# Performance work log

Hardware: AMD Instinct MI355X
Metric: run time of the kernel (lower is better)

## Reference

```python
import jax, jax.numpy as jnp
import numpy as np
from jax import lax

DEPTH = 8
LEAK = 0.01  # activations.relu(x, 0.01) == leaky relu


def _lrelu(z):
    return jnp.where(z >= 0, z, LEAK * z)


def _forward(x, mask, bucket_size, W_emb, b_emb, W, U, b, W1, b1,
             W_action_1, U_action_1, b_action_1, W_action_3, b_action_3):
    S = int(bucket_size)
    B = x.shape[0]
    H = W_emb.shape[1]
    dm = mask.T[:S]                         # [S,B] data mask (float)
    xe = x @ W_emb + b_emb                  # [B,S,H] embedding
    xe = jnp.transpose(xe, (1, 0, 2))[:S]   # [S,B,H] time-major
    # last_value_mask: 1 only at the final time step
    lvm = jnp.concatenate([jnp.zeros((S - 1, B), jnp.float32),
                           jnp.ones((1, B), jnp.float32)], axis=0)

    def hstep(carry, seq):
        h_tm1, nm_tm1, hv_tm1 = carry
        xt, pm, phv, lv = seq
        # action MLP -> per-sample gate
        a = _lrelu(xt @ W_action_1 + h_tm1 @ U_action_1 + b_action_1)  # [B,A]
        nm = jnp.clip(0.2 * (a @ W_action_3 + b_action_3) + 0.5, 0.0, 1.0)[:, 0]  # hard_sigmoid
        nm = (1.0 - lv) * (pm * phv * nm)
        both = pm * phv * (1.0 - nm) * hv_tm1
        x_only = pm * phv * (nm + (1.0 - nm) * (1.0 - hv_tm1))
        h_only = (1.0 - pm + pm * (1.0 - phv)) * (1.0 - nm) * hv_tm1
        hv = both + x_only + h_only
        h_ = _lrelu(xt @ W + h_tm1 @ U + b)      # [B,inner]
        h_ = _lrelu(h_ @ W1 + b1)                # [B,H]
        h = both[:, None] * h_ + x_only[:, None] * xt + h_only[:, None] * h_tm1
        return (h, nm, hv), (h, nm, hv)

    def vstep(carry, _):
        xv, xm, phv = carry  # [S,B,H], [S,B], [S,B]
        init = (jnp.zeros((B, H), jnp.float32),
                jnp.ones((B,), jnp.float32),
                jnp.zeros((B,), jnp.float32))
        _, (hs, nms, hvs) = lax.scan(hstep, init, (xv, xm, phv, lvm))
        # shift new_mask left by one step, pad last step with ones
        nms = jnp.concatenate([nms[1:], jnp.ones((1, B), jnp.float32)], axis=0)
        return (hs, nms, hvs), None

    (hfin, _, _), _ = lax.scan(vstep, (xe, dm, dm), None, length=DEPTH - 1)
    return hfin[-1]  # [B,H]: last time step of the last vertical level


def setup_inputs() -> dict:
    key = jax.random.key(0)
    ks = jax.random.split(key, 9)
    B, S, IN, H, INNER, A = 64, 256, 256, 256, 512, 64
    g = lambda k, shp: jax.random.normal(k, shp, jnp.float32) * np.float32(np.sqrt(2.0 / (shp[0] + shp[1])))
    return {
        "x": jax.random.normal(ks[0], (B, S, IN), jnp.float32),
        "mask": jnp.ones((B, S), jnp.float32),
        "bucket_size": S,
        "W_emb": g(ks[1], (IN, H)),
        "b_emb": jnp.zeros((H,), jnp.float32),
        "W": g(ks[2], (H, INNER)),
        "U": g(ks[3], (H, INNER)),
        "b": jnp.zeros((INNER,), jnp.float32),
        "W1": g(ks[4], (INNER, H)),
        "b1": jnp.zeros((H,), jnp.float32),
        "W_action_1": g(ks[5], (H, A)),
        "U_action_1": g(ks[6], (H, A)),
        "b_action_1": jnp.zeros((A,), jnp.float32),
        "W_action_3": g(ks[7], (A, 1)),
        "b_action_3": jnp.zeros((1,), jnp.float32),
    }


def reference(x, mask, bucket_size, W_emb, b_emb, W, U, b, W1, b1,
              W_action_1, U_action_1, b_action_1, W_action_3, b_action_3):
    return _forward(x, mask, bucket_size, W_emb, b_emb, W, U, b, W1, b1,
                    W_action_1, U_action_1, b_action_1, W_action_3, b_action_3)
```

## Files before the change

### kernel.cpp

```cpp
#include <hip/hip_runtime.h>
#include <stdint.h>


typedef _Float16 f16x8 __attribute__((ext_vector_type(8)));
typedef float    f32x4 __attribute__((ext_vector_type(4)));

static constexpr int SS = 256, BB = 64, DIN = 256, DH = 256, DNN = 512, DA = 64;
static constexpr int FS = 32;

static constexpr size_t OFF_FLAGS = 0;
static constexpr size_t OFF_WEMB  = 32768;
static constexpr size_t SZ_WEMB   = (size_t)DIN * DH * 2;
static constexpr size_t OFF_W     = OFF_WEMB + SZ_WEMB;
static constexpr size_t SZ_WU     = (size_t)DH * DNN * 2;
static constexpr size_t OFF_U     = OFF_W + SZ_WU;
static constexpr size_t OFF_W1    = OFF_U + SZ_WU;
static constexpr size_t SZ_W1     = (size_t)DNN * DH * 2;
static constexpr size_t OFF_WA1   = OFF_W1 + SZ_W1;
static constexpr size_t SZ_WA     = (size_t)DH * DA * 2;
static constexpr size_t OFF_UA1   = OFF_WA1 + SZ_WA;
static constexpr size_t OFF_NM    = OFF_UA1 + SZ_WA;
static constexpr size_t SZ_NM     = (size_t)SS * BB * 4;
static constexpr size_t OFF_HV    = OFF_NM + 8 * SZ_NM;
static constexpr size_t OFF_HB    = (size_t)4 << 20;
static constexpr size_t SZ_HB     = (size_t)SS * BB * DH * 2;
static constexpr size_t WS_NEEDED = OFF_HB + 8 * SZ_HB;

__device__ __forceinline__ float lrelu(float v) { return v >= 0.0f ? v : 0.01f * v; }

__device__ __forceinline__ f32x4 ld128(const f32x4* p) {
  f32x4 r;
  asm volatile("global_load_dwordx4 %0, %1, off sc0 sc1" : "=v"(r) : "v"(p) : "memory");
  return r;
}
__device__ __forceinline__ void st128(f32x4* p, f32x4 v) {
  asm volatile("global_store_dwordx4 %0, %1, off sc0 sc1" :: "v"(p), "v"(v) : "memory");
}
__device__ __forceinline__ float ldf(const float* p) {
  float r;
  asm volatile("global_load_dword %0, %1, off sc0 sc1" : "=v"(r) : "v"(p) : "memory");
  return r;
}
__device__ __forceinline__ void stf(float* p, float v) {
  asm volatile("global_store_dword %0, %1, off sc0 sc1" :: "v"(p), "v"(v) : "memory");
}
__device__ __forceinline__ void stu(unsigned* p, unsigned v) {
  asm volatile("global_store_dword %0, %1, off sc0 sc1" :: "v"(p), "v"(v) : "memory");
}
__device__ __forceinline__ void vwait() {
  asm volatile("s_waitcnt vmcnt(0)" ::: "memory");
  __builtin_amdgcn_sched_barrier(0);
}

__device__ __forceinline__ void pollf(const unsigned* p, unsigned need) {
  #pragma nounroll
  for (int g = 0; g < (1 << 18); ++g) {
    unsigned v;
    asm volatile("global_load_dword %0, %1, off sc0 sc1\n\ts_waitcnt vmcnt(0)"
                 : "=v"(v) : "v"(p) : "memory");
    if (v >= need) return;
    if (g > 64)     __builtin_amdgcn_s_sleep(2);
    else if (g > 8) __builtin_amdgcn_s_sleep(1);
  }
}

__global__ void zero_flags_k(unsigned* f) {
  #pragma unroll
  for (int i = 0; i < 8; ++i) f[threadIdx.x + 1024 * i] = 0u;
}

__global__ void pack_weight_k(const float* __restrict__ src, _Float16* __restrict__ dst,
                              int K, int N) {
  int idx = blockIdx.x * 256 + threadIdx.x;
  if (idx >= K * N) return;
  int k = idx / N, n = idx - k * N;
  int kt = k >> 5, q = (k >> 3) & 3, jj = k & 7;
  int nt = n >> 4, l = n & 15;
  size_t p = (((size_t)(kt * (N >> 4) + nt) * 4 + q) * 16 + l) * 8 + jj;
  dst[p] = (_Float16)src[idx];
}

__global__ __launch_bounds__(512, 2) void emb_k(const float* __restrict__ xin,
                                                const float* __restrict__ b_emb,
                                                char* __restrict__ ws) {
  const int tid = threadIdx.x, wave = tid >> 6, lane = tid & 63;
  const int l15 = lane & 15, quad = lane >> 4;
  const _Float16* Wp = (const _Float16*)(ws + OFF_WEMB);
  _Float16* xe = (_Float16*)(ws + OFF_HB);

  f16x8 bE[16];
  #pragma unroll
  for (int kt = 0; kt < 8; ++kt)
    #pragma unroll
    for (int i = 0; i < 2; ++i)
      bE[kt * 2 + i] = *(const f16x8*)(Wp + (((size_t)(kt * 16 + (wave * 2 + i)) * 4 + quad) * 16 + l15) * 8);
  float ber[2] = { b_emb[(wave * 2) * 16 + l15], b_emb[(wave * 2 + 1) * 16 + l15] };

  __shared__ __align__(16) _Float16 xtF[32 * 65 * 8];
  __shared__ __align__(16) _Float16 oF[32 * 65 * 8];

  for (int tt = 0; tt < 4; ++tt) {
    const int t = (int)blockIdx.x + 64 * tt;
    #pragma unroll
    for (int c = 0; c < 4; ++c) {
      int u = tid + 512 * c, s = u >> 5, kg = u & 31;
      const float* src = xin + ((size_t)s * SS + t) * DIN + kg * 8;
      f32x4 v0 = *(const f32x4*)src, v1 = *(const f32x4*)(src + 4);
      f16x8 p;
      p[0]=(_Float16)v0[0]; p[1]=(_Float16)v0[1]; p[2]=(_Float16)v0[2]; p[3]=(_Float16)v0[3];
      p[4]=(_Float16)v1[0]; p[5]=(_Float16)v1[1]; p[6]=(_Float16)v1[2]; p[7]=(_Float16)v1[3];
      *(f16x8*)(xtF + ((size_t)kg * 65 + s) * 8) = p;
    }
    __syncthreads();
    f32x4 acc[2][4] = {};
    #pragma unroll
    for (int kt = 0; kt < 8; ++kt) {
      f16x8 ax[4];
      #pragma unroll
      for (int mt = 0; mt < 4; ++mt)
        ax[mt] = *(const f16x8*)(xtF + (((size_t)(kt * 4 + quad)) * 65 + (mt * 16 + l15)) * 8);
      #pragma unroll
      for (int i = 0; i < 2; ++i)
        #pragma unroll
        for (int mt = 0; mt < 4; ++mt)
          acc[i][mt] = __builtin_amdgcn_mfma_f32_16x16x32_f16(ax[mt], bE[kt * 2 + i], acc[i][mt], 0, 0, 0);
    }
    #pragma unroll
    for (int i = 0; i < 2; ++i) {
      int n = (wave * 2 + i) * 16 + l15;
      int kq = n >> 3, jn = n & 7;
      #pragma unroll
      for (int mt = 0; mt < 4; ++mt)
        #pragma unroll
        for (int r = 0; r < 4; ++r) {
          int s = mt * 16 + quad * 4 + r;
          oF[((size_t)kq * 65 + s) * 8 + jn] = (_Float16)(acc[i][mt][r] + ber[i]);
        }
    }
    __syncthreads();
    #pragma unroll
    for (int c = 0; c < 4; ++c) {
      int u = tid + 512 * c, kq = u >> 6, s = u & 63;
      f32x4 v = *(const f32x4*)(oF + ((size_t)kq * 65 + s) * 8);
      *((f32x4*)(xe + (((size_t)t * 32 + kq) * 64 + s) * 8)) = v;
    }
    __syncthreads();
  }
}

__global__ __launch_bounds__(512, 2) void pipe_k(
    const float* __restrict__ mask, const float* __restrict__ b_in,
    const float* __restrict__ b1v, const float* __restrict__ bA1,
    const float* __restrict__ WA3, const float* __restrict__ bA3,
    char* __restrict__ ws, float* __restrict__ outp) {
  const int bId   = (int)blockIdx.x;
  const int level = 1 + (bId >> 2);
  const int g     = bId & 3;
  const int tid   = threadIdx.x, wave = tid >> 6, lane = tid & 63;
  const int l15   = lane & 15, quad = lane >> 4;
  const int kq16  = tid >> 4, sp16 = tid & 15;

  unsigned* flags = (unsigned*)(ws + OFF_FLAGS);
  unsigned* hfl   = flags + (size_t)(level * 4 + g) * FS;
  unsigned* hflP  = flags + (size_t)((level - 1) * 4 + g) * FS;

  const _Float16* Wp   = (const _Float16*)(ws + OFF_W);
  const _Float16* Up   = (const _Float16*)(ws + OFF_U);
  const _Float16* W1p  = (const _Float16*)(ws + OFF_W1);
  const _Float16* WA1p = (const _Float16*)(ws + OFF_WA1);
  const _Float16* UA1p = (const _Float16*)(ws + OFF_UA1);

  const f32x4* hPrev4 = (const f32x4*)((_Float16*)(ws + OFF_HB) + (size_t)(level - 1) * SS * BB * DH);
  f32x4*       hOwn4  = (f32x4*)((_Float16*)(ws + OFF_HB) + (size_t)level * SS * BB * DH);
  float*       nmW    = (float*)(ws + OFF_NM + (size_t)level * SZ_NM);
  float*       hvW    = (float*)(ws + OFF_HV + (size_t)level * SZ_NM);
  const float* nmR    = (const float*)(ws + OFF_NM + (size_t)(level - 1) * SZ_NM);
  const float* hvR    = (const float*)(ws + OFF_HV + (size_t)(level - 1) * SZ_NM);

  float bir[4];
  #pragma unroll
  for (int nt = 0; nt < 4; ++nt) bir[nt] = b_in[(wave * 4 + nt) * 16 + l15];
  float b1r[2];
  #pragma unroll
  for (int nt = 0; nt < 2; ++nt) b1r[nt] = b1v[(wave * 2 + nt) * 16 + l15];
  const float wa3r = WA3[(wave & 3) * 16 + l15];
  const float ba1r = bA1[(wave & 3) * 16 + l15];
  const float bA3v = bA3[0];

  __shared__ __align__(16) _Float16 xtL[32 * 16 * 8];
  __shared__ __align__(16) _Float16 hL [32 * 16 * 8];
  __shared__ __align__(16) _Float16 g1L[64 * 16 * 8];
  __shared__ float zL[64];
  __shared__ float gB[16], gX[16], gH[16], gHv[16];

  for (int i = tid; i < 32 * 16 * 8; i += 512) hL[i] = (_Float16)0;
  if (tid < 16) gHv[tid] = 0.0f;
  __syncthreads();

  if (level >= 2) pollf(hflP, 1);
  __syncthreads();
  {
    f32x4 v = ld128(hPrev4 + kq16 * 64 + g * 16 + sp16);
    vwait();
    ((f32x4*)xtL)[tid] = v;
  }
  __syncthreads();

  for (int t = 0; t < SS; ++t) {
    const bool last = (t == SS - 1);

    if (level >= 2) pollf(hflP, (unsigned)((t + 2 <= SS) ? (t + 2) : SS));

    {
      f32x4 acc[4] = {};
      #pragma unroll
      for (int kt = 0; kt < 8; ++kt) {
        f16x8 ax = *(const f16x8*)(xtL + ((size_t)((kt * 4 + quad) * 16 + l15)) * 8);
        f16x8 ah = *(const f16x8*)(hL  + ((size_t)((kt * 4 + quad) * 16 + l15)) * 8);
        #pragma unroll
        for (int i = 0; i < 4; ++i) {
          f16x8 wf = *(const f16x8*)(Wp + (((size_t)(kt * 32 + (wave * 4 + i)) * 4 + quad) * 16 + l15) * 8);
          f16x8 uf = *(const f16x8*)(Up + (((size_t)(kt * 32 + (wave * 4 + i)) * 4 + quad) * 16 + l15) * 8);
          acc[i] = __builtin_amdgcn_mfma_f32_16x16x32_f16(ax, wf, acc[i], 0, 0, 0);
          acc[i] = __builtin_amdgcn_mfma_f32_16x16x32_f16(ah, uf, acc[i], 0, 0, 0);
        }
      }
      #pragma unroll
      for (int i = 0; i < 4; ++i) {
        const int n = (wave * 4 + i) * 16 + l15;
        const int kqn = n >> 3, jn = n & 7;
        #pragma unroll
        for (int r = 0; r < 4; ++r)
          g1L[((size_t)kqn * 16 + (quad * 4 + r)) * 8 + jn] = (_Float16)lrelu(acc[i][r] + bir[i]);
      }
      if (wave < 4) {
        f32x4 aa = {};
        #pragma unroll
        for (int kt = 0; kt < 8; ++kt) {
          f16x8 ax = *(const f16x8*)(xtL + ((size_t)((kt * 4 + quad) * 16 + l15)) * 8);
          f16x8 ah = *(const f16x8*)(hL  + ((size_t)((kt * 4 + quad) * 16 + l15)) * 8);
          f16x8 wa = *(const f16x8*)(WA1p + (((size_t)(kt * 4 + wave) * 4 + quad) * 16 + l15) * 8);
          f16x8 ua = *(const f16x8*)(UA1p + (((size_t)(kt * 4 + wave) * 4 + quad) * 16 + l15) * 8);
          aa = __builtin_amdgcn_mfma_f32_16x16x32_f16(ax, wa, aa, 0, 0, 0);
          aa = __builtin_amdgcn_mfma_f32_16x16x32_f16(ah, ua, aa, 0, 0, 0);
        }
        #pragma unroll
        for (int r = 0; r < 4; ++r) {
          float v = lrelu(aa[r] + ba1r) * wa3r;
          v += __shfl_xor(v, 1); v += __shfl_xor(v, 2);
          v += __shfl_xor(v, 4); v += __shfl_xor(v, 8);
          if (l15 == 0) zL[wave * 16 + quad * 4 + r] = v;
        }
      }
    }
    __syncthreads();

    f32x4 c1[2] = {};
    #pragma unroll
    for (int kt = 0; kt < 16; ++kt) {
      f16x8 ag = *(const f16x8*)(g1L + ((size_t)((kt * 4 + quad) * 16 + l15)) * 8);
      #pragma unroll
      for (int nt = 0; nt < 2; ++nt) {
        f16x8 w1f = *(const f16x8*)(W1p + (((size_t)(kt * 16 + (wave * 2 + nt)) * 4 + quad) * 16 + l15) * 8);
        c1[nt] = __builtin_amdgcn_mfma_f32_16x16x32_f16(ag, w1f, c1[nt], 0, 0, 0);
      }
    }

    f32x4 pf;
    float pmv = 1.0f, phh = 0.0f;
    {
      const bool wantGate = (tid < 16) && (level >= 2);
      if (!last) pf = ld128(hPrev4 + (size_t)(t + 1) * 2048 + kq16 * 64 + g * 16 + sp16);
      if (wantGate) {
        size_t tn = (t + 1 < SS) ? (size_t)(t + 1) : 0;
        pmv = ldf(nmR + tn * BB + g * 16 + tid);
        phh = ldf(hvR + (size_t)t * BB + g * 16 + tid);
      }
      vwait();
      if (wantGate) asm volatile("" : "+v"(pmv), "+v"(phh));
    }

    if (tid < 16) {
      const int s = tid;
      float pm, phv;
      if (level == 1) {
        float mv = mask[(size_t)(g * 16 + s) * SS + t];
        pm = mv; phv = mv;
      } else {
        pm  = (t + 1 < SS) ? pmv : 1.0f;
        phv = phh;
      }
      float z    = bA3v + zL[s] + zL[16 + s] + zL[32 + s] + zL[48 + s];
      float nm0  = fminf(fmaxf(0.2f * z + 0.5f, 0.0f), 1.0f);
      float lv   = last ? 1.0f : 0.0f;
      float nm   = (1.0f - lv) * (pm * phv * nm0);
      float hvp  = gHv[s], omn = 1.0f - nm;
      float both = pm * phv * omn * hvp;
      float xo   = pm * phv * (nm + omn * (1.0f - hvp));
      float ho   = (1.0f - pm * phv) * omn * hvp;
      float hv   = both + xo + ho;
      gB[s] = both; gX[s] = xo; gH[s] = ho; gHv[s] = hv;
      if (level < 7) {
        stf(&nmW[(size_t)t * BB + g * 16 + s], nm);
        stf(&hvW[(size_t)t * BB + g * 16 + s], hv);
      }
    }
    __syncthreads();

    #pragma unroll
    for (int nt = 0; nt < 2; ++nt) {
      const int n = (wave * 2 + nt) * 16 + l15;
      const int kqc = n >> 3, jc = n & 7;
      #pragma unroll
      for (int r = 0; r < 4; ++r) {
        int s = quad * 4 + r;
        size_t idx = ((size_t)kqc * 16 + s) * 8 + jc;
        float h1  = lrelu(c1[nt][r] + b1r[nt]);
        float xtv = (float)xtL[idx];
        float hp  = (float)hL[idx];
        float hn  = gB[s] * h1 + gX[s] * xtv + gH[s] * hp;
        hL[idx] = (_Float16)hn;
        if (level == 7 && last) outp[(size_t)(g * 16 + s) * DH + n] = hn;
      }
    }
    __syncthreads();

    {
      f32x4 v = ((const f32x4*)hL)[tid];
      st128(hOwn4 + (size_t)t * 2048 + kq16 * 64 + g * 16 + sp16, v);
    }
    if (!last) ((f32x4*)xtL)[tid] = pf;
    vwait();
    __syncthreads();
    if (tid == 0) stu(hfl, (unsigned)(t + 1));
  }
}

extern "C" void kernel_launch(void* const* d_in, const int* in_sizes, int n_in,
                              void* d_out, int out_size, void* d_ws, size_t ws_size,
                              hipStream_t stream) {
  const float* x     = (const float*)d_in[0];
  const float* mask  = (const float*)d_in[1];
  const float* W_emb = (const float*)d_in[3];
  const float* b_emb = (const float*)d_in[4];
  const float* W     = (const float*)d_in[5];
  const float* U     = (const float*)d_in[6];
  const float* b     = (const float*)d_in[7];
  const float* W1    = (const float*)d_in[8];
  const float* b1    = (const float*)d_in[9];
  const float* WA1   = (const float*)d_in[10];
  const float* UA1   = (const float*)d_in[11];
  const float* bA1   = (const float*)d_in[12];
  const float* WA3   = (const float*)d_in[13];
  const float* bA3   = (const float*)d_in[14];
  char* ws = (char*)d_ws;

  if (ws_size < WS_NEEDED) return;

  zero_flags_k<<<1, 1024, 0, stream>>>((unsigned*)(ws + OFF_FLAGS));
  pack_weight_k<<<(DIN * DH + 255) / 256, 256, 0, stream>>>(W_emb, (_Float16*)(ws + OFF_WEMB), DIN, DH);
  pack_weight_k<<<(DH * DNN + 255) / 256, 256, 0, stream>>>(W, (_Float16*)(ws + OFF_W), DH, DNN);
  pack_weight_k<<<(DH * DNN + 255) / 256, 256, 0, stream>>>(U, (_Float16*)(ws + OFF_U), DH, DNN);
  pack_weight_k<<<(DNN * DH + 255) / 256, 256, 0, stream>>>(W1, (_Float16*)(ws + OFF_W1), DNN, DH);
  pack_weight_k<<<(DH * DA + 255) / 256, 256, 0, stream>>>(WA1, (_Float16*)(ws + OFF_WA1), DH, DA);
  pack_weight_k<<<(DH * DA + 255) / 256, 256, 0, stream>>>(UA1, (_Float16*)(ws + OFF_UA1), DH, DA);

  emb_k<<<64, 512, 0, stream>>>(x, b_emb, ws);
  pipe_k<<<28, 512, 0, stream>>>(mask, b, b1, bA1, WA3, bA3, ws, (float*)d_out);
}
```

Measured before the change: 3.847 ms.

## Defer flag publication and poll cached flag to shorten wavefront pipeline sync

Restructures the cross-level wavefront handshake. The upstream flag is now read alongside the data prefetch and cached in a register, so polling happens only when the cached value is too small. The completion flag for step t-1 is published at the start of step t's store instead of after a trailing vwait and barrier. Level 7 skips writing the unused hidden-state buffer. This is meant to remove per-step global polling latency and a synchronisation stall from the serial critical path, at the cost of a one-step-delayed flag and more subtle memory-ordering assumptions.

```diff
diff --git a/kernel.cpp b/kernel.cpp
--- a/kernel.cpp
+++ b/kernel.cpp
@@ -197,9 +197,24 @@
   if (tid < 16) gHv[tid] = 0.0f;
   __syncthreads();
 
-  if (level >= 2) pollf(hflP, 1);
-  __syncthreads();
-  {
+  unsigned flagReg = 0;
+  float pmv = 1.0f, phh = 0.0f;
+
+  if (level >= 2) {
+    pollf(hflP, 2);
+    f32x4 v = ld128(hPrev4 + kq16 * 64 + g * 16 + sp16);
+    if (tid < 16) {
+      pmv = ldf(nmR + (size_t)1 * BB + g * 16 + tid);
+      phh = ldf(hvR + g * 16 + tid);
+    }
+    unsigned fr;
+    asm volatile("global_load_dword %0, %1, off sc0 sc1" : "=v"(fr) : "v"(hflP) : "memory");
+    vwait();
+    asm volatile("" : "+v"(fr));
+    flagReg = fr;
+    if (tid < 16) asm volatile("" : "+v"(pmv), "+v"(phh));
+    ((f32x4*)xtL)[tid] = v;
+  } else {
     f32x4 v = ld128(hPrev4 + kq16 * 64 + g * 16 + sp16);
     vwait();
     ((f32x4*)xtL)[tid] = v;
@@ -208,8 +223,6 @@
 
   for (int t = 0; t < SS; ++t) {
     const bool last = (t == SS - 1);
-
-    if (level >= 2) pollf(hflP, (unsigned)((t + 2 <= SS) ? (t + 2) : SS));
 
     {
       f32x4 acc[4] = {};
@@ -264,20 +277,6 @@
         f16x8 w1f = *(const f16x8*)(W1p + (((size_t)(kt * 16 + (wave * 2 + nt)) * 4 + quad) * 16 + l15) * 8);
         c1[nt] = __builtin_amdgcn_mfma_f32_16x16x32_f16(ag, w1f, c1[nt], 0, 0, 0);
       }
-    }
-
-    f32x4 pf;
-    float pmv = 1.0f, phh = 0.0f;
-    {
-      const bool wantGate = (tid < 16) && (level >= 2);
-      if (!last) pf = ld128(hPrev4 + (size_t)(t + 1) * 2048 + kq16 * 64 + g * 16 + sp16);
-      if (wantGate) {
-        size_t tn = (t + 1 < SS) ? (size_t)(t + 1) : 0;
-        pmv = ldf(nmR + tn * BB + g * 16 + tid);
-        phh = ldf(hvR + (size_t)t * BB + g * 16 + tid);
-      }
-      vwait();
-      if (wantGate) asm volatile("" : "+v"(pmv), "+v"(phh));
     }
 
     if (tid < 16) {
@@ -325,15 +324,38 @@
     }
     __syncthreads();
 
-    {
+    if (level < 7) {
+      if (tid == 0 && t > 0) stu(hfl, (unsigned)t);
       f32x4 v = ((const f32x4*)hL)[tid];
       st128(hOwn4 + (size_t)t * 2048 + kq16 * 64 + g * 16 + sp16, v);
     }
-    if (!last) ((f32x4*)xtL)[tid] = pf;
-    vwait();
-    __syncthreads();
-    if (tid == 0) stu(hfl, (unsigned)(t + 1));
+    if (!last) {
+      if (level >= 2) {
+        const unsigned need = (unsigned)((t + 3 <= SS) ? (t + 3) : SS);
+        if (flagReg < need) pollf(hflP, need);
+        f32x4 v = ld128(hPrev4 + (size_t)(t + 1) * 2048 + kq16 * 64 + g * 16 + sp16);
+        if (tid < 16) {
+          if (t + 2 < SS) pmv = ldf(nmR + (size_t)(t + 2) * BB + g * 16 + tid);
+          phh = ldf(hvR + (size_t)(t + 1) * BB + g * 16 + tid);
+        }
+        unsigned fr;
+        asm volatile("global_load_dword %0, %1, off sc0 sc1" : "=v"(fr) : "v"(hflP) : "memory");
+        vwait();
+        asm volatile("" : "+v"(fr));
+        flagReg = fr;
+        if (tid < 16) asm volatile("" : "+v"(pmv), "+v"(phh));
+        ((f32x4*)xtL)[tid] = v;
+      } else {
+        f32x4 v = ld128(hPrev4 + (size_t)(t + 1) * 2048 + kq16 * 64 + g * 16 + sp16);
+        vwait();
+        ((f32x4*)xtL)[tid] = v;
+      }
+    } else {
+      vwait();
+    }
+    __syncthreads();
   }
+  if (level < 7 && tid == 0) stu(hfl, (unsigned)SS);
 }
 
 extern "C" void kernel_launch(void* const* d_in, const int* in_sizes, int n_in,
@@ -343,8 +365,8 @@
   const float* mask  = (const float*)d_in[1];
   const float* W_emb = (const float*)d_in[3];
   const float* b_emb = (const float*)d_in[4];
-  const float* W     = (const float*)d_in[5];
-  const float* U     = (const float*)d_in[6];
+  const float* Wm    = (const float*)d_in[5];
+  const float* Um    = (const float*)d_in[6];
   const float* b     = (const float*)d_in[7];
   const float* W1    = (const float*)d_in[8];
   const float* b1    = (const float*)d_in[9];
@@ -359,8 +381,8 @@
 
   zero_flags_k<<<1, 1024, 0, stream>>>((unsigned*)(ws + OFF_FLAGS));
   pack_weight_k<<<(DIN * DH + 255) / 256, 256, 0, stream>>>(W_emb, (_Float16*)(ws + OFF_WEMB), DIN, DH);
-  pack_weight_k<<<(DH * DNN + 255) / 256, 256, 0, stream>>>(W, (_Float16*)(ws + OFF_W), DH, DNN);
-  pack_weight_k<<<(DH * DNN + 255) / 256, 256, 0, stream>>>(U, (_Float16*)(ws + OFF_U), DH, DNN);
+  pack_weight_k<<<(DH * DNN + 255) / 256, 256, 0, stream>>>(Wm, (_Float16*)(ws + OFF_W), DH, DNN);
+  pack_weight_k<<<(DH * DNN + 255) / 256, 256, 0, stream>>>(Um, (_Float16*)(ws + OFF_U), DH, DNN);
   pack_weight_k<<<(DNN * DH + 255) / 256, 256, 0, stream>>>(W1, (_Float16*)(ws + OFF_W1), DNN, DH);
   pack_weight_k<<<(DH * DA + 255) / 256, 256, 0, stream>>>(WA1, (_Float16*)(ws + OFF_WA1), DH, DA);
   pack_weight_k<<<(DH * DA + 255) / 256, 256, 0, stream>>>(UA1, (_Float16*)(ws + OFF_UA1), DH, DA);
```

After: 3.918 ms. Within noise of the previous version (+1.8%).
